# Kernel optimization log

Measured on AMD Instinct MI355X. Metric: run time of the kernel, lower is better.

## Reference

```python
import jax, jax.numpy as jnp
import numpy as np

N, M1, M2, D, S0, S1 = 60000, 40000, 40000, 64, 10, 20

def setup_inputs() -> dict:
    key = jax.random.key(0)
    ks = jax.random.split(key, 10)
    return {
        "h0": jax.random.normal(ks[0], (N, D), jnp.float32),
        "h1": jax.random.normal(ks[1], (M1, D), jnp.float32),
        "h2": jax.random.normal(ks[2], (M2, D), jnp.float32),
        "nei0": jax.random.randint(ks[3], (N, S0), 0, M1),
        "nei1": jax.random.randint(ks[4], (N, S1), 0, M2),
        "att_w0": jax.random.normal(ks[5], (1, 2 * D), jnp.float32) * 0.15,
        "att_w1": jax.random.normal(ks[6], (1, 2 * D), jnp.float32) * 0.15,
        "fc_w": jax.random.normal(ks[7], (D, D), jnp.float32) * 0.15,
        "fc_b": jnp.zeros((D,), jnp.float32),
        "fus_att_w": jax.random.normal(ks[8], (1, D), jnp.float32) * 0.15,
        "glob_att": jax.random.normal(ks[9], (1, D), jnp.float32) * 0.15,
        "gate": jnp.float32(0.8),
    }

def _nei_att(nei, h, h_refer, att_w):
    # F.embedding gather: [N, S, D]
    nei_emb = h[nei]
    d = h.shape[-1]
    # concat([h_refer, nei_emb]) @ att.T == h_refer@a_ref + nei_emb@a_nei
    a_ref, a_nei = att_w[0, :d], att_w[0, d:]
    scores = (h_refer @ a_ref)[:, None] + nei_emb @ a_nei  # [N, S]
    scores = jax.nn.leaky_relu(scores, 0.01)
    w = jax.nn.softmax(scores, axis=1)  # softmax over neighbors
    return jnp.einsum('ns,nsd->nd', w, nei_emb)

def reference(h0, h1, h2, nei0, nei1, att_w0, att_w1, fc_w, fc_b, fus_att_w, glob_att, gate):
    # intra (per neighbor type) attention + elu
    e0 = jax.nn.elu(_nei_att(nei0, h1, h0, att_w0))
    e1 = jax.nn.elu(_nei_att(nei1, h2, h0, att_w1))
    # fus_att (inter-type semantic attention)
    def beta_of(e):
        sp = jnp.tanh(e @ fc_w.T + fc_b)
        return (sp @ fus_att_w[0]).mean()
    beta = jax.nn.softmax(jnp.stack([beta_of(e0), beta_of(e1)]))
    z_mc = beta[0] * e0 + beta[1] * e1
    # global encoder: softmax over all nodes of all types
    all_nodes = jnp.concatenate([h0, h1, h2], axis=0)
    s = (all_nodes @ glob_att[0]) / jnp.sqrt(jnp.float32(D))
    w = jax.nn.softmax(s, axis=0)[:, None]
    global_embed = (w * all_nodes).sum(axis=0)  # [D]
    # weighted gate fusion
    gv = jax.nn.sigmoid(gate)
    return gv * z_mc + (1.0 - gv) * global_embed
```

## Files before the change

### kernel.cpp

```cpp
#include <hip/hip_runtime.h>
#include <math.h>

#define N_NODES 60000
#define M1_N    40000
#define M2_N    40000
#define DD      64
#define S0_N    10
#define S1_N    20
#define R_TOTAL (N_NODES + M1_N + M2_N)
#define T_H0    (N_NODES / 16)
#define T_H1    (T_H0 + M1_N / 16)
#define T_ALL   (T_H1 + M2_N / 16)
#define PROJ_GRID 1024
#define BETA_GRID 512

typedef __attribute__((ext_vector_type(8))) short short8;
typedef __attribute__((ext_vector_type(4))) float f32x4;

__device__ __forceinline__ float wave_sum(float x) {
#pragma unroll
    for (int o = 32; o >= 1; o >>= 1) x += __shfl_xor(x, o, 64);
    return x;
}
__device__ __forceinline__ float bcast(float v, int l) {
    return __uint_as_float(__builtin_amdgcn_readlane(__float_as_uint(v), l));
}
__device__ __forceinline__ float tanh_fast(float x) {
    return 1.f - 2.f / (__expf(2.f * x) + 1.f);
}
__device__ __forceinline__ unsigned short f2bf(float x) {
    unsigned u = __float_as_uint(x);
    return (unsigned short)((u + 0x7FFFu + ((u >> 16) & 1u)) >> 16);
}
__device__ __forceinline__ float bf2f(unsigned short u) {
    return __uint_as_float(((unsigned)u) << 16);
}

__global__ __launch_bounds__(256) void k_proj(
    const float* __restrict__ h0, const float* __restrict__ h1, const float* __restrict__ h2,
    const float* __restrict__ aw0, const float* __restrict__ aw1, const float* __restrict__ gatt,
    float* __restrict__ part,
    float* __restrict__ p0r0, float* __restrict__ p0r1,
    float* __restrict__ p1, float* __restrict__ p2,
    unsigned short* __restrict__ h1bf, unsigned short* __restrict__ h2bf)
{
    __shared__ float s_wsum[64];
    __shared__ float s_se;
    __shared__ float s_es[4][16];
    const int tid = threadIdx.x, lane = tid & 63, wid = tid >> 6;
    if (tid < 64) s_wsum[tid] = 0.f;
    if (tid == 0) s_se = 0.f;
    __syncthreads();

    const int m = lane & 15, quad = lane >> 4;

    short8 b0, b1;
    {
        const float* vsel = 0;
        if (m == 1) vsel = aw0;
        else if (m == 2) vsel = aw1;
        else if (m == 3) vsel = aw0 + DD;
        else if (m == 4) vsel = aw1 + DD;
        else if (m == 0) vsel = gatt;
#pragma unroll
        for (int j = 0; j < 8; j++) {
            b0[j] = vsel ? (short)f2bf(vsel[quad * 8 + j]) : (short)0;
            b1[j] = vsel ? (short)f2bf(vsel[32 + quad * 8 + j]) : (short)0;
        }
    }

    float wacc0[8], wacc1[8];
#pragma unroll
    for (int j = 0; j < 8; j++) { wacc0[j] = 0.f; wacc1[j] = 0.f; }
    float r_se = 0.f;

    const int gw = blockIdx.x * 4 + wid, nw = gridDim.x * 4;
    for (int tile = gw; tile < T_ALL; tile += nw) {
        const float* src; int rbase, region;
        if (tile < T_H0)      { src = h0; rbase = tile * 16;          region = 0; }
        else if (tile < T_H1) { src = h1; rbase = (tile - T_H0) * 16; region = 1; }
        else                  { src = h2; rbase = (tile - T_H1) * 16; region = 2; }
        const int row = rbase + m;
        const float4* rpa = (const float4*)(src + (size_t)row * DD + quad * 8);
        const float4* rpb = (const float4*)(src + (size_t)row * DD + 32 + quad * 8);
        const float4 va = rpa[0], vb = rpa[1];
        const float4 vc = rpb[0], vd = rpb[1];

        short8 a0, a1;
        a0[0] = (short)f2bf(va.x); a0[1] = (short)f2bf(va.y);
        a0[2] = (short)f2bf(va.z); a0[3] = (short)f2bf(va.w);
        a0[4] = (short)f2bf(vb.x); a0[5] = (short)f2bf(vb.y);
        a0[6] = (short)f2bf(vb.z); a0[7] = (short)f2bf(vb.w);
        a1[0] = (short)f2bf(vc.x); a1[1] = (short)f2bf(vc.y);
        a1[2] = (short)f2bf(vc.z); a1[3] = (short)f2bf(vc.w);
        a1[4] = (short)f2bf(vd.x); a1[5] = (short)f2bf(vd.y);
        a1[6] = (short)f2bf(vd.z); a1[7] = (short)f2bf(vd.w);

        f32x4 c = {0.f, 0.f, 0.f, 0.f};
        c = __builtin_amdgcn_mfma_f32_16x16x32_bf16(a0, b0, c, 0, 0, 0);
        c = __builtin_amdgcn_mfma_f32_16x16x32_bf16(a1, b1, c, 0, 0, 0);

        if (m == 0) {
            float4 e4;
            e4.x = __expf(c[0] * 0.125f); e4.y = __expf(c[1] * 0.125f);
            e4.z = __expf(c[2] * 0.125f); e4.w = __expf(c[3] * 0.125f);
            *(float4*)&s_es[wid][quad * 4] = e4;
        }
        __builtin_amdgcn_wave_barrier();
        const float es = s_es[wid][m];
        r_se += es;
        wacc0[0] = fmaf(es, va.x, wacc0[0]); wacc0[1] = fmaf(es, va.y, wacc0[1]);
        wacc0[2] = fmaf(es, va.z, wacc0[2]); wacc0[3] = fmaf(es, va.w, wacc0[3]);
        wacc0[4] = fmaf(es, vb.x, wacc0[4]); wacc0[5] = fmaf(es, vb.y, wacc0[5]);
        wacc0[6] = fmaf(es, vb.z, wacc0[6]); wacc0[7] = fmaf(es, vb.w, wacc0[7]);
        wacc1[0] = fmaf(es, vc.x, wacc1[0]); wacc1[1] = fmaf(es, vc.y, wacc1[1]);
        wacc1[2] = fmaf(es, vc.z, wacc1[2]); wacc1[3] = fmaf(es, vc.w, wacc1[3]);
        wacc1[4] = fmaf(es, vd.x, wacc1[4]); wacc1[5] = fmaf(es, vd.y, wacc1[5]);
        wacc1[6] = fmaf(es, vd.z, wacc1[6]); wacc1[7] = fmaf(es, vd.w, wacc1[7]);

        if (region == 0) {
            if (m == 1) { float4 t = {c[0], c[1], c[2], c[3]}; *(float4*)(p0r0 + rbase + quad * 4) = t; }
            if (m == 2) { float4 t = {c[0], c[1], c[2], c[3]}; *(float4*)(p0r1 + rbase + quad * 4) = t; }
        } else if (region == 1) {
            if (m == 3) { float4 t = {c[0], c[1], c[2], c[3]}; *(float4*)(p1 + rbase + quad * 4) = t; }
            *(short8*)(h1bf + (size_t)row * DD + quad * 8) = a0;
            *(short8*)(h1bf + (size_t)row * DD + 32 + quad * 8) = a1;
        } else {
            if (m == 4) { float4 t = {c[0], c[1], c[2], c[3]}; *(float4*)(p2 + rbase + quad * 4) = t; }
            *(short8*)(h2bf + (size_t)row * DD + quad * 8) = a0;
            *(short8*)(h2bf + (size_t)row * DD + 32 + quad * 8) = a1;
        }
    }

    r_se *= 0.25f;
#pragma unroll
    for (int o = 1; o <= 8; o <<= 1) {
#pragma unroll
        for (int j = 0; j < 8; j++) {
            wacc0[j] += __shfl_xor(wacc0[j], o, 64);
            wacc1[j] += __shfl_xor(wacc1[j], o, 64);
        }
    }
    if (m == 0) {
#pragma unroll
        for (int j = 0; j < 8; j++) {
            atomicAdd(&s_wsum[quad * 8 + j],      wacc0[j]);
            atomicAdd(&s_wsum[32 + quad * 8 + j], wacc1[j]);
        }
    }
    const float se = wave_sum(r_se);
    if (lane == 0) atomicAdd(&s_se, se);
    __syncthreads();
    if (tid < 64) part[tid * PROJ_GRID + blockIdx.x] = s_wsum[tid];
    if (tid == 64) part[64 * PROJ_GRID + blockIdx.x] = s_se;
}

__global__ __launch_bounds__(256) void k_attn(
    const unsigned short* __restrict__ h1bf, const unsigned short* __restrict__ h2bf,
    const int* __restrict__ nei0, const int* __restrict__ nei1,
    const float* __restrict__ p0r0, const float* __restrict__ p0r1,
    const float* __restrict__ p1, const float* __restrict__ p2,
    unsigned short* __restrict__ e0bf, unsigned short* __restrict__ e1bf)
{
    const int tid = threadIdx.x, lane = tid & 63, wid = tid >> 6;
    const bool grp0 = (lane < S0_N);
    const bool grp1 = (lane >= 32) && (lane < 32 + S1_N);
    const int gw = blockIdx.x * 4 + wid;
    const int nw = gridDim.x * 4;
    for (int n = gw; n < N_NODES; n += nw) {
        const float pr0 = p0r0[n];
        const float pr1 = p0r1[n];

        int idx = 0; float w = 0.f;
        if (grp0) idx = nei0[n * S0_N + lane];
        if (grp1) idx = nei1[n * S1_N + (lane - 32)];
        if (grp0 | grp1) {
            float t = (grp0 ? pr0 : pr1) + (grp0 ? p1[idx] : p2[idx]);
            t = (t >= 0.f) ? t : 0.01f * t;
            w = __expf(t);
        }
        float sv = w;
#pragma unroll
        for (int o = 16; o >= 1; o >>= 1) sv += __shfl_xor(sv, o, 64);
        const float inv0 = 1.f / bcast(sv, 0);
        const float inv1 = 1.f / bcast(sv, 32);

        float v0[S0_N], v1[S1_N];
#pragma unroll
        for (int s = 0; s < S0_N; s++) {
            const int i0 = __builtin_amdgcn_readlane(idx, s);
            v0[s] = bf2f(h1bf[i0 * DD + lane]);
        }
#pragma unroll
        for (int s = 0; s < S1_N; s++) {
            const int i1 = __builtin_amdgcn_readlane(idx, 32 + s);
            v1[s] = bf2f(h2bf[i1 * DD + lane]);
        }

        {
            float ea = 0.f, eb = 0.f;
#pragma unroll
            for (int s = 0; s < S0_N; s += 2) {
                ea = fmaf(bcast(w, s),     v0[s],     ea);
                eb = fmaf(bcast(w, s + 1), v0[s + 1], eb);
            }
            float e = (ea + eb) * inv0;
            e = (e > 0.f) ? e : (__expf(e) - 1.f);
            e0bf[n * DD + lane] = f2bf(e);
        }
        {
            float ea = 0.f, eb = 0.f, ec = 0.f, ed = 0.f;
#pragma unroll
            for (int s = 0; s < S1_N; s += 4) {
                ea = fmaf(bcast(w, 32 + s), v1[s],     ea);
                eb = fmaf(bcast(w, 33 + s), v1[s + 1], eb);
                ec = fmaf(bcast(w, 34 + s), v1[s + 2], ec);
                ed = fmaf(bcast(w, 35 + s), v1[s + 3], ed);
            }
            float e = ((ea + eb) + (ec + ed)) * inv1;
            e = (e > 0.f) ? e : (__expf(e) - 1.f);
            e1bf[n * DD + lane] = f2bf(e);
        }
    }
}

__global__ __launch_bounds__(256) void k_beta(
    const unsigned short* __restrict__ e0bf, const unsigned short* __restrict__ e1bf,
    const float* __restrict__ fcw, const float* __restrict__ fcb,
    const float* __restrict__ fus, float* __restrict__ bpart)
{
    __shared__ float s_part[2];
    const int tid = threadIdx.x, lane = tid & 63, wid = tid >> 6;
    if (tid < 2) s_part[tid] = 0.f;
    const int m = lane & 15, q = lane >> 4;

    short8 bfr[4][2];
    float fb[4], fu[4];
#pragma unroll
    for (int t = 0; t < 4; t++) {
        const float* wrow = fcw + (t * 16 + m) * DD;
#pragma unroll
        for (int h = 0; h < 2; h++) {
            const float* p = wrow + h * 32 + q * 8;
#pragma unroll
            for (int j = 0; j < 8; j++) bfr[t][h][j] = (short)f2bf(p[j]);
        }
        fb[t] = fcb[t * 16 + m];
        fu[t] = fus[t * 16 + m];
    }
    __syncthreads();

    float rb0 = 0.f, rb1 = 0.f;
    const int gw = blockIdx.x * 4 + wid;
    const int nw = gridDim.x * 4;
    for (int tile = gw; tile < N_NODES / 16; tile += nw) {
        const int rowbase = (tile * 16 + m) * DD + q * 8;
        {
            const short8 a0 = *(const short8*)(e0bf + rowbase);
            const short8 a1 = *(const short8*)(e0bf + rowbase + 32);
            f32x4 c[4];
#pragma unroll
            for (int t = 0; t < 4; t++) {
                c[t] = f32x4{0.f, 0.f, 0.f, 0.f};
                c[t] = __builtin_amdgcn_mfma_f32_16x16x32_bf16(a0, bfr[t][0], c[t], 0, 0, 0);
                c[t] = __builtin_amdgcn_mfma_f32_16x16x32_bf16(a1, bfr[t][1], c[t], 0, 0, 0);
            }
#pragma unroll
            for (int t = 0; t < 4; t++)
#pragma unroll
                for (int j = 0; j < 4; j++)
                    rb0 += tanh_fast(c[t][j] + fb[t]) * fu[t];
        }
        {
            const short8 a0 = *(const short8*)(e1bf + rowbase);
            const short8 a1 = *(const short8*)(e1bf + rowbase + 32);
            f32x4 c[4];
#pragma unroll
            for (int t = 0; t < 4; t++) {
                c[t] = f32x4{0.f, 0.f, 0.f, 0.f};
                c[t] = __builtin_amdgcn_mfma_f32_16x16x32_bf16(a0, bfr[t][0], c[t], 0, 0, 0);
                c[t] = __builtin_amdgcn_mfma_f32_16x16x32_bf16(a1, bfr[t][1], c[t], 0, 0, 0);
            }
#pragma unroll
            for (int t = 0; t < 4; t++)
#pragma unroll
                for (int j = 0; j < 4; j++)
                    rb1 += tanh_fast(c[t][j] + fb[t]) * fu[t];
        }
    }
    const float b0 = wave_sum(rb0);
    const float b1 = wave_sum(rb1);
    if (lane == 0) { atomicAdd(&s_part[0], b0); atomicAdd(&s_part[1], b1); }
    __syncthreads();
    if (tid == 0) {
        bpart[blockIdx.x]             = s_part[0];
        bpart[BETA_GRID + blockIdx.x] = s_part[1];
    }
}

__global__ __launch_bounds__(256) void k_reduce(
    const float* __restrict__ part, const float* __restrict__ bpart,
    float* __restrict__ accum)
{
    const int tid = threadIdx.x, lane = tid & 63, wid = tid >> 6;
    if (wid == 0) {
        float t0 = 0.f, t1 = 0.f;
#pragma unroll
        for (int k = 0; k < BETA_GRID / 64; k++) {
            t0 += bpart[lane + 64 * k];
            t1 += bpart[BETA_GRID + lane + 64 * k];
        }
        t0 = wave_sum(t0); t1 = wave_sum(t1);
        if (lane == 0) { accum[0] = t0; accum[1] = t1; }
    }
    for (int j = wid; j < 65; j += 4) {
        float s = 0.f;
#pragma unroll
        for (int k = 0; k < PROJ_GRID / 64; k++)
            s += part[j * PROJ_GRID + lane + 64 * k];
        s = wave_sum(s);
        if (lane == 0) {
            if (j < 64) accum[4 + j] = s;
            else        accum[2] = s;
        }
    }
}

__global__ __launch_bounds__(256) void k_out(
    const unsigned short* __restrict__ e0bf, const unsigned short* __restrict__ e1bf,
    const float* __restrict__ accum, const float* __restrict__ gate,
    float* __restrict__ out)
{
    const int i = blockIdx.x * 256 + threadIdx.x;
    const float b0 = accum[0] * (1.f / N_NODES);
    const float b1 = accum[1] * (1.f / N_NODES);
    const float mx = fmaxf(b0, b1);
    const float eb0 = __expf(b0 - mx), eb1 = __expf(b1 - mx);
    const float gv  = 1.f / (1.f + __expf(-gate[0]));
    const float c0  = gv * eb0 / (eb0 + eb1);
    const float c1  = gv * eb1 / (eb0 + eb1);
    const float cg  = (1.f - gv) / accum[2];

    const float4 av = ((const float4*)(accum + 4))[i & 15];
    const ushort4 ua = ((const ushort4*)e0bf)[i];
    const ushort4 ub = ((const ushort4*)e1bf)[i];
    float4 o;
    o.x = c0 * bf2f(ua.x) + c1 * bf2f(ub.x) + cg * av.x;
    o.y = c0 * bf2f(ua.y) + c1 * bf2f(ub.y) + cg * av.y;
    o.z = c0 * bf2f(ua.z) + c1 * bf2f(ub.z) + cg * av.z;
    o.w = c0 * bf2f(ua.w) + c1 * bf2f(ub.w) + cg * av.w;
    ((float4*)out)[i] = o;
}

extern "C" void kernel_launch(void* const* d_in, const int* in_sizes, int n_in,
                              void* d_out, int out_size, void* d_ws, size_t ws_size,
                              hipStream_t stream) {
    (void)in_sizes; (void)n_in; (void)out_size; (void)ws_size;
    const float* h0   = (const float*)d_in[0];
    const float* h1   = (const float*)d_in[1];
    const float* h2   = (const float*)d_in[2];
    const int*   nei0 = (const int*)  d_in[3];
    const int*   nei1 = (const int*)  d_in[4];
    const float* aw0  = (const float*)d_in[5];
    const float* aw1  = (const float*)d_in[6];
    const float* fcw  = (const float*)d_in[7];
    const float* fcb  = (const float*)d_in[8];
    const float* fus  = (const float*)d_in[9];
    const float* gatt = (const float*)d_in[10];
    const float* gate = (const float*)d_in[11];
    float* out = (float*)d_out;

    float* ws    = (float*)d_ws;
    float* accum = ws;
    float* p0r0  = ws + 256;
    float* p0r1  = p0r0 + N_NODES;
    float* p1    = p0r1 + N_NODES;
    float* p2    = p1 + M1_N;
    unsigned short* h1bf = (unsigned short*)(p2 + M2_N);
    unsigned short* h2bf = h1bf + (size_t)M1_N * DD;
    unsigned short* e0bf = h2bf + (size_t)M2_N * DD;
    unsigned short* e1bf = e0bf + (size_t)N_NODES * DD;
    float* part  = (float*)(e1bf + (size_t)N_NODES * DD);
    float* bpart = part + 65 * PROJ_GRID;

    k_proj<<<PROJ_GRID, 256, 0, stream>>>(h0, h1, h2, aw0, aw1, gatt, part,
                                          p0r0, p0r1, p1, p2, h1bf, h2bf);
    k_attn<<<2048, 256, 0, stream>>>(h1bf, h2bf, nei0, nei1, p0r0, p0r1, p1, p2, e0bf, e1bf);
    k_beta<<<BETA_GRID, 256, 0, stream>>>(e0bf, e1bf, fcw, fcb, fus, bpart);
    k_reduce<<<1, 256, 0, stream>>>(part, bpart, accum);
    k_out<<<(N_NODES * DD / 4) / 256, 256, 0, stream>>>(e0bf, e1bf, accum, gate, out);
}
```

Baseline: 176.9 us.

## Fuse beta projection into attention kernel via per-wave LDS tiles

Merges the separate semantic-attention (beta) kernel into the neighbour-attention kernel. Each wave now processes a 16-node tile, stages its bf16 e0/e1 rows in LDS and runs the MFMA fc projection plus tanh reduction directly. This removes the global re-read of e0bf/e1bf and one kernel launch. The h2/p2 gathers are also addressed through h1bf/p1 with an M1 offset, relying on the buffers being laid out contiguously in the workspace. In exchange the grid shrinks to 960 blocks and each wave loops serially over 16 nodes, which lowers the number of waves available to hide gather latency.

```diff
diff --git a/kernel.cpp b/kernel.cpp
--- a/kernel.cpp
+++ b/kernel.cpp
@@ -12,7 +12,8 @@
 #define T_H1    (T_H0 + M1_N / 16)
 #define T_ALL   (T_H1 + M2_N / 16)
 #define PROJ_GRID 1024
-#define BETA_GRID 512
+#define ATTN_GRID 960
+#define N_TILES  (N_NODES / 16)
 
 typedef __attribute__((ext_vector_type(8))) short short8;
 typedef __attribute__((ext_vector_type(4))) float f32x4;
@@ -156,136 +157,126 @@
 }
 
 __global__ __launch_bounds__(256) void k_attn(
-    const unsigned short* __restrict__ h1bf, const unsigned short* __restrict__ h2bf,
+    const unsigned short* __restrict__ h1bf,
     const int* __restrict__ nei0, const int* __restrict__ nei1,
     const float* __restrict__ p0r0, const float* __restrict__ p0r1,
-    const float* __restrict__ p1, const float* __restrict__ p2,
-    unsigned short* __restrict__ e0bf, unsigned short* __restrict__ e1bf)
+    const float* __restrict__ p1,
+    const float* __restrict__ fcw, const float* __restrict__ fcb,
+    const float* __restrict__ fus,
+    unsigned short* __restrict__ e0bf, unsigned short* __restrict__ e1bf,
+    float* __restrict__ bpart)
 {
-    const int tid = threadIdx.x, lane = tid & 63, wid = tid >> 6;
-    const bool grp0 = (lane < S0_N);
-    const bool grp1 = (lane >= 32) && (lane < 32 + S1_N);
-    const int gw = blockIdx.x * 4 + wid;
-    const int nw = gridDim.x * 4;
-    for (int n = gw; n < N_NODES; n += nw) {
-        const float pr0 = p0r0[n];
-        const float pr1 = p0r1[n];
-
-        int idx = 0; float w = 0.f;
-        if (grp0) idx = nei0[n * S0_N + lane];
-        if (grp1) idx = nei1[n * S1_N + (lane - 32)];
-        if (grp0 | grp1) {
-            float t = (grp0 ? pr0 : pr1) + (grp0 ? p1[idx] : p2[idx]);
-            t = (t >= 0.f) ? t : 0.01f * t;
-            w = __expf(t);
-        }
-        float sv = w;
-#pragma unroll
-        for (int o = 16; o >= 1; o >>= 1) sv += __shfl_xor(sv, o, 64);
-        const float inv0 = 1.f / bcast(sv, 0);
-        const float inv1 = 1.f / bcast(sv, 32);
-
-        float v0[S0_N], v1[S1_N];
-#pragma unroll
-        for (int s = 0; s < S0_N; s++) {
-            const int i0 = __builtin_amdgcn_readlane(idx, s);
-            v0[s] = bf2f(h1bf[i0 * DD + lane]);
-        }
-#pragma unroll
-        for (int s = 0; s < S1_N; s++) {
-            const int i1 = __builtin_amdgcn_readlane(idx, 32 + s);
-            v1[s] = bf2f(h2bf[i1 * DD + lane]);
-        }
-
-        {
-            float ea = 0.f, eb = 0.f;
-#pragma unroll
-            for (int s = 0; s < S0_N; s += 2) {
-                ea = fmaf(bcast(w, s),     v0[s],     ea);
-                eb = fmaf(bcast(w, s + 1), v0[s + 1], eb);
-            }
-            float e = (ea + eb) * inv0;
-            e = (e > 0.f) ? e : (__expf(e) - 1.f);
-            e0bf[n * DD + lane] = f2bf(e);
-        }
-        {
-            float ea = 0.f, eb = 0.f, ec = 0.f, ed = 0.f;
-#pragma unroll
-            for (int s = 0; s < S1_N; s += 4) {
-                ea = fmaf(bcast(w, 32 + s), v1[s],     ea);
-                eb = fmaf(bcast(w, 33 + s), v1[s + 1], eb);
-                ec = fmaf(bcast(w, 34 + s), v1[s + 2], ec);
-                ed = fmaf(bcast(w, 35 + s), v1[s + 3], ed);
-            }
-            float e = ((ea + eb) + (ec + ed)) * inv1;
-            e = (e > 0.f) ? e : (__expf(e) - 1.f);
-            e1bf[n * DD + lane] = f2bf(e);
-        }
-    }
-}
-
-__global__ __launch_bounds__(256) void k_beta(
-    const unsigned short* __restrict__ e0bf, const unsigned short* __restrict__ e1bf,
-    const float* __restrict__ fcw, const float* __restrict__ fcb,
-    const float* __restrict__ fus, float* __restrict__ bpart)
-{
+    __shared__ __align__(16) unsigned short s_et[4][2][16 * 88];
     __shared__ float s_part[2];
     const int tid = threadIdx.x, lane = tid & 63, wid = tid >> 6;
     if (tid < 2) s_part[tid] = 0.f;
-    const int m = lane & 15, q = lane >> 4;
+    const int m = lane & 15, quad = lane >> 4;
 
     short8 bfr[4][2];
     float fb[4], fu[4];
 #pragma unroll
-    for (int t = 0; t < 4; t++) {
-        const float* wrow = fcw + (t * 16 + m) * DD;
+    for (int t4 = 0; t4 < 4; t4++) {
+        const float* wrow = fcw + (t4 * 16 + m) * DD;
 #pragma unroll
         for (int h = 0; h < 2; h++) {
-            const float* p = wrow + h * 32 + q * 8;
-#pragma unroll
-            for (int j = 0; j < 8; j++) bfr[t][h][j] = (short)f2bf(p[j]);
-        }
-        fb[t] = fcb[t * 16 + m];
-        fu[t] = fus[t * 16 + m];
+            const float* p = wrow + h * 32 + quad * 8;
+#pragma unroll
+            for (int j = 0; j < 8; j++) bfr[t4][h][j] = (short)f2bf(p[j]);
+        }
+        fb[t4] = fcb[t4 * 16 + m];
+        fu[t4] = fus[t4 * 16 + m];
     }
     __syncthreads();
 
     float rb0 = 0.f, rb1 = 0.f;
-    const int gw = blockIdx.x * 4 + wid;
-    const int nw = gridDim.x * 4;
-    for (int tile = gw; tile < N_NODES / 16; tile += nw) {
-        const int rowbase = (tile * 16 + m) * DD + q * 8;
-        {
-            const short8 a0 = *(const short8*)(e0bf + rowbase);
-            const short8 a1 = *(const short8*)(e0bf + rowbase + 32);
+    const int t = blockIdx.x * 4 + wid;
+    if (t < N_TILES) {
+        const bool grp0 = (lane < S0_N);
+        const bool grp1 = (lane >= 32) && (lane < 32 + S1_N);
+#pragma unroll 1
+        for (int i = 0; i < 16; i++) {
+            const int n = t * 16 + i;
+            const float pr0 = p0r0[n];
+            const float pr1 = p0r1[n];
+
+            int idx = 0; float w = 0.f;
+            if (grp0) idx = nei0[n * S0_N + lane];
+            if (grp1) idx = nei1[n * S1_N + (lane - 32)] + M1_N;
+            if (grp0 | grp1) {
+                float sc = (grp0 ? pr0 : pr1) + p1[idx];
+                sc = (sc >= 0.f) ? sc : 0.01f * sc;
+                w = __expf(sc);
+            }
+
+            float v0[S0_N], v1[S1_N];
+#pragma unroll
+            for (int s = 0; s < S0_N; s++) {
+                const int i0 = __builtin_amdgcn_readlane(idx, s);
+                v0[s] = bf2f(h1bf[i0 * DD + lane]);
+            }
+#pragma unroll
+            for (int s = 0; s < S1_N; s++) {
+                const int i1 = __builtin_amdgcn_readlane(idx, 32 + s);
+                v1[s] = bf2f(h1bf[i1 * DD + lane]);
+            }
+
+            float sv = w;
+#pragma unroll
+            for (int o = 16; o >= 1; o >>= 1) sv += __shfl_xor(sv, o, 64);
+            const float inv0 = 1.f / bcast(sv, 0);
+            const float inv1 = 1.f / bcast(sv, 32);
+
+            float e0v, e1v;
+            {
+                float ea = 0.f, eb = 0.f;
+#pragma unroll
+                for (int s = 0; s < S0_N; s += 2) {
+                    ea = fmaf(bcast(w, s),     v0[s],     ea);
+                    eb = fmaf(bcast(w, s + 1), v0[s + 1], eb);
+                }
+                float e = (ea + eb) * inv0;
+                e0v = (e > 0.f) ? e : (__expf(e) - 1.f);
+            }
+            {
+                float ea = 0.f, eb = 0.f, ec = 0.f, ed = 0.f;
+#pragma unroll
+                for (int s = 0; s < S1_N; s += 4) {
+                    ea = fmaf(bcast(w, 32 + s), v1[s],     ea);
+                    eb = fmaf(bcast(w, 33 + s), v1[s + 1], eb);
+                    ec = fmaf(bcast(w, 34 + s), v1[s + 2], ec);
+                    ed = fmaf(bcast(w, 35 + s), v1[s + 3], ed);
+                }
+                float e = ((ea + eb) + (ec + ed)) * inv1;
+                e1v = (e > 0.f) ? e : (__expf(e) - 1.f);
+            }
+            const unsigned short bs0 = f2bf(e0v);
+            const unsigned short bs1 = f2bf(e1v);
+            e0bf[n * DD + lane] = bs0;
+            e1bf[n * DD + lane] = bs1;
+            s_et[wid][0][i * 88 + lane] = bs0;
+            s_et[wid][1][i * 88 + lane] = bs1;
+        }
+        __builtin_amdgcn_wave_barrier();
+
+#pragma unroll
+        for (int which = 0; which < 2; which++) {
+            const unsigned short* bp = &s_et[wid][which][m * 88 + quad * 8];
+            const short8 a0 = *(const short8*)bp;
+            const short8 a1 = *(const short8*)(bp + 32);
             f32x4 c[4];
 #pragma unroll
-            for (int t = 0; t < 4; t++) {
-                c[t] = f32x4{0.f, 0.f, 0.f, 0.f};
-                c[t] = __builtin_amdgcn_mfma_f32_16x16x32_bf16(a0, bfr[t][0], c[t], 0, 0, 0);
-                c[t] = __builtin_amdgcn_mfma_f32_16x16x32_bf16(a1, bfr[t][1], c[t], 0, 0, 0);
-            }
-#pragma unroll
-            for (int t = 0; t < 4; t++)
+            for (int t4 = 0; t4 < 4; t4++) {
+                c[t4] = f32x4{0.f, 0.f, 0.f, 0.f};
+                c[t4] = __builtin_amdgcn_mfma_f32_16x16x32_bf16(a0, bfr[t4][0], c[t4], 0, 0, 0);
+                c[t4] = __builtin_amdgcn_mfma_f32_16x16x32_bf16(a1, bfr[t4][1], c[t4], 0, 0, 0);
+            }
+            float r = 0.f;
+#pragma unroll
+            for (int t4 = 0; t4 < 4; t4++)
 #pragma unroll
                 for (int j = 0; j < 4; j++)
-                    rb0 += tanh_fast(c[t][j] + fb[t]) * fu[t];
-        }
-        {
-            const short8 a0 = *(const short8*)(e1bf + rowbase);
-            const short8 a1 = *(const short8*)(e1bf + rowbase + 32);
-            f32x4 c[4];
-#pragma unroll
-            for (int t = 0; t < 4; t++) {
-                c[t] = f32x4{0.f, 0.f, 0.f, 0.f};
-                c[t] = __builtin_amdgcn_mfma_f32_16x16x32_bf16(a0, bfr[t][0], c[t], 0, 0, 0);
-                c[t] = __builtin_amdgcn_mfma_f32_16x16x32_bf16(a1, bfr[t][1], c[t], 0, 0, 0);
-            }
-#pragma unroll
-            for (int t = 0; t < 4; t++)
-#pragma unroll
-                for (int j = 0; j < 4; j++)
-                    rb1 += tanh_fast(c[t][j] + fb[t]) * fu[t];
+                    r += tanh_fast(c[t4][j] + fb[t4]) * fu[t4];
+            if (which == 0) rb0 = r; else rb1 = r;
         }
     }
     const float b0 = wave_sum(rb0);
@@ -294,7 +285,7 @@
     __syncthreads();
     if (tid == 0) {
         bpart[blockIdx.x]             = s_part[0];
-        bpart[BETA_GRID + blockIdx.x] = s_part[1];
+        bpart[ATTN_GRID + blockIdx.x] = s_part[1];
     }
 }
 
@@ -306,9 +297,9 @@
     if (wid == 0) {
         float t0 = 0.f, t1 = 0.f;
 #pragma unroll
-        for (int k = 0; k < BETA_GRID / 64; k++) {
+        for (int k = 0; k < ATTN_GRID / 64; k++) {
             t0 += bpart[lane + 64 * k];
-            t1 += bpart[BETA_GRID + lane + 64 * k];
+            t1 += bpart[ATTN_GRID + lane + 64 * k];
         }
         t0 = wave_sum(t0); t1 = wave_sum(t1);
         if (lane == 0) { accum[0] = t0; accum[1] = t1; }
@@ -385,8 +376,8 @@
 
     k_proj<<<PROJ_GRID, 256, 0, stream>>>(h0, h1, h2, aw0, aw1, gatt, part,
                                           p0r0, p0r1, p1, p2, h1bf, h2bf);
-    k_attn<<<2048, 256, 0, stream>>>(h1bf, h2bf, nei0, nei1, p0r0, p0r1, p1, p2, e0bf, e1bf);
-    k_beta<<<BETA_GRID, 256, 0, stream>>>(e0bf, e1bf, fcw, fcb, fus, bpart);
+    k_attn<<<ATTN_GRID, 256, 0, stream>>>(h1bf, nei0, nei1, p0r0, p0r1, p1,
+                                          fcw, fcb, fus, e0bf, e1bf, bpart);
     k_reduce<<<1, 256, 0, stream>>>(part, bpart, accum);
     k_out<<<(N_NODES * DD / 4) / 256, 256, 0, stream>>>(e0bf, e1bf, accum, gate, out);
 }
```

Measured after the change: 196.6 us. 11.1% more time.

## Gather neighbor rows with 8-byte vector loads, four rows per wave instruction

Applied to the files above, without the earlier changes.

The attention kernel now splits each wave into four 16-lane groups. Each lane loads four bf16 values of one neighbor row at once, so one instruction fetches four rows, instead of one scalar bf16 per lane per neighbor. Weighted sums are built per group and combined with cross-group shuffles; group 0 writes e0 and group 1 writes e1 as ushort4 stores. It also treats h2bf and p2 as a tail of h1bf and p1 by offsetting nei1 indices by M1, which relies on the workspace keeping those buffers contiguous. The goal is fewer memory instructions and wider transactions in a latency-bound gather, at the cost of extra shuffles and padded zero-weight lanes.

```diff
diff --git a/kernel.cpp b/kernel.cpp
--- a/kernel.cpp
+++ b/kernel.cpp
@@ -156,13 +156,14 @@
 }
 
 __global__ __launch_bounds__(256) void k_attn(
-    const unsigned short* __restrict__ h1bf, const unsigned short* __restrict__ h2bf,
+    const unsigned short* __restrict__ h1bf,
     const int* __restrict__ nei0, const int* __restrict__ nei1,
     const float* __restrict__ p0r0, const float* __restrict__ p0r1,
-    const float* __restrict__ p1, const float* __restrict__ p2,
+    const float* __restrict__ p1,
     unsigned short* __restrict__ e0bf, unsigned short* __restrict__ e1bf)
 {
     const int tid = threadIdx.x, lane = tid & 63, wid = tid >> 6;
+    const int sub = lane & 15, grp = lane >> 4;
     const bool grp0 = (lane < S0_N);
     const bool grp1 = (lane >= 32) && (lane < 32 + S1_N);
     const int gw = blockIdx.x * 4 + wid;
@@ -173,53 +174,79 @@
 
         int idx = 0; float w = 0.f;
         if (grp0) idx = nei0[n * S0_N + lane];
-        if (grp1) idx = nei1[n * S1_N + (lane - 32)];
+        if (grp1) idx = nei1[n * S1_N + (lane - 32)] + M1_N;
         if (grp0 | grp1) {
-            float t = (grp0 ? pr0 : pr1) + (grp0 ? p1[idx] : p2[idx]);
-            t = (t >= 0.f) ? t : 0.01f * t;
-            w = __expf(t);
-        }
+            float sc = (grp0 ? pr0 : pr1) + p1[idx];
+            sc = (sc >= 0.f) ? sc : 0.01f * sc;
+            w = __expf(sc);
+        }
+
+        int r0[3], r1[5];
+#pragma unroll
+        for (int j = 0; j < 3; j++) r0[j] = __shfl(idx, 4 * j + grp, 64);
+#pragma unroll
+        for (int j = 0; j < 5; j++) r1[j] = __shfl(idx, 32 + 4 * j + grp, 64);
+
+        ushort4 u0[3], u1[5];
+#pragma unroll
+        for (int j = 0; j < 3; j++)
+            u0[j] = *(const ushort4*)(h1bf + r0[j] * DD + 4 * sub);
+#pragma unroll
+        for (int j = 0; j < 5; j++)
+            u1[j] = *(const ushort4*)(h1bf + r1[j] * DD + 4 * sub);
+
         float sv = w;
 #pragma unroll
         for (int o = 16; o >= 1; o >>= 1) sv += __shfl_xor(sv, o, 64);
         const float inv0 = 1.f / bcast(sv, 0);
         const float inv1 = 1.f / bcast(sv, 32);
 
-        float v0[S0_N], v1[S1_N];
-#pragma unroll
-        for (int s = 0; s < S0_N; s++) {
-            const int i0 = __builtin_amdgcn_readlane(idx, s);
-            v0[s] = bf2f(h1bf[i0 * DD + lane]);
-        }
-#pragma unroll
-        for (int s = 0; s < S1_N; s++) {
-            const int i1 = __builtin_amdgcn_readlane(idx, 32 + s);
-            v1[s] = bf2f(h2bf[i1 * DD + lane]);
-        }
-
-        {
-            float ea = 0.f, eb = 0.f;
-#pragma unroll
-            for (int s = 0; s < S0_N; s += 2) {
-                ea = fmaf(bcast(w, s),     v0[s],     ea);
-                eb = fmaf(bcast(w, s + 1), v0[s + 1], eb);
-            }
-            float e = (ea + eb) * inv0;
-            e = (e > 0.f) ? e : (__expf(e) - 1.f);
-            e0bf[n * DD + lane] = f2bf(e);
-        }
-        {
-            float ea = 0.f, eb = 0.f, ec = 0.f, ed = 0.f;
-#pragma unroll
-            for (int s = 0; s < S1_N; s += 4) {
-                ea = fmaf(bcast(w, 32 + s), v1[s],     ea);
-                eb = fmaf(bcast(w, 33 + s), v1[s + 1], eb);
-                ec = fmaf(bcast(w, 34 + s), v1[s + 2], ec);
-                ed = fmaf(bcast(w, 35 + s), v1[s + 3], ed);
-            }
-            float e = ((ea + eb) + (ec + ed)) * inv1;
-            e = (e > 0.f) ? e : (__expf(e) - 1.f);
-            e1bf[n * DD + lane] = f2bf(e);
+        float w0[3], w1[5];
+#pragma unroll
+        for (int j = 0; j < 3; j++) w0[j] = __shfl(w, 4 * j + grp, 64);
+#pragma unroll
+        for (int j = 0; j < 5; j++) w1[j] = __shfl(w, 32 + 4 * j + grp, 64);
+
+        float4 a0 = make_float4(0.f, 0.f, 0.f, 0.f);
+#pragma unroll
+        for (int j = 0; j < 3; j++) {
+            a0.x = fmaf(w0[j], bf2f(u0[j].x), a0.x);
+            a0.y = fmaf(w0[j], bf2f(u0[j].y), a0.y);
+            a0.z = fmaf(w0[j], bf2f(u0[j].z), a0.z);
+            a0.w = fmaf(w0[j], bf2f(u0[j].w), a0.w);
+        }
+        float4 a1 = make_float4(0.f, 0.f, 0.f, 0.f);
+#pragma unroll
+        for (int j = 0; j < 5; j++) {
+            a1.x = fmaf(w1[j], bf2f(u1[j].x), a1.x);
+            a1.y = fmaf(w1[j], bf2f(u1[j].y), a1.y);
+            a1.z = fmaf(w1[j], bf2f(u1[j].z), a1.z);
+            a1.w = fmaf(w1[j], bf2f(u1[j].w), a1.w);
+        }
+#pragma unroll
+        for (int o = 16; o <= 32; o <<= 1) {
+            a0.x += __shfl_xor(a0.x, o, 64); a0.y += __shfl_xor(a0.y, o, 64);
+            a0.z += __shfl_xor(a0.z, o, 64); a0.w += __shfl_xor(a0.w, o, 64);
+            a1.x += __shfl_xor(a1.x, o, 64); a1.y += __shfl_xor(a1.y, o, 64);
+            a1.z += __shfl_xor(a1.z, o, 64); a1.w += __shfl_xor(a1.w, o, 64);
+        }
+        float4 e0v, e1v;
+        e0v.x = a0.x * inv0; e0v.y = a0.y * inv0; e0v.z = a0.z * inv0; e0v.w = a0.w * inv0;
+        e1v.x = a1.x * inv1; e1v.y = a1.y * inv1; e1v.z = a1.z * inv1; e1v.w = a1.w * inv1;
+        e0v.x = (e0v.x > 0.f) ? e0v.x : (__expf(e0v.x) - 1.f);
+        e0v.y = (e0v.y > 0.f) ? e0v.y : (__expf(e0v.y) - 1.f);
+        e0v.z = (e0v.z > 0.f) ? e0v.z : (__expf(e0v.z) - 1.f);
+        e0v.w = (e0v.w > 0.f) ? e0v.w : (__expf(e0v.w) - 1.f);
+        e1v.x = (e1v.x > 0.f) ? e1v.x : (__expf(e1v.x) - 1.f);
+        e1v.y = (e1v.y > 0.f) ? e1v.y : (__expf(e1v.y) - 1.f);
+        e1v.z = (e1v.z > 0.f) ? e1v.z : (__expf(e1v.z) - 1.f);
+        e1v.w = (e1v.w > 0.f) ? e1v.w : (__expf(e1v.w) - 1.f);
+        if (grp == 0) {
+            ushort4 s; s.x = f2bf(e0v.x); s.y = f2bf(e0v.y); s.z = f2bf(e0v.z); s.w = f2bf(e0v.w);
+            *(ushort4*)(e0bf + n * DD + 4 * sub) = s;
+        } else if (grp == 1) {
+            ushort4 s; s.x = f2bf(e1v.x); s.y = f2bf(e1v.y); s.z = f2bf(e1v.z); s.w = f2bf(e1v.w);
+            *(ushort4*)(e1bf + n * DD + 4 * sub) = s;
         }
     }
 }
@@ -385,7 +412,7 @@
 
     k_proj<<<PROJ_GRID, 256, 0, stream>>>(h0, h1, h2, aw0, aw1, gatt, part,
                                           p0r0, p0r1, p1, p2, h1bf, h2bf);
-    k_attn<<<2048, 256, 0, stream>>>(h1bf, h2bf, nei0, nei1, p0r0, p0r1, p1, p2, e0bf, e1bf);
+    k_attn<<<2048, 256, 0, stream>>>(h1bf, nei0, nei1, p0r0, p0r1, p1, e0bf, e1bf);
     k_beta<<<BETA_GRID, 256, 0, stream>>>(e0bf, e1bf, fcw, fcb, fus, bpart);
     k_reduce<<<1, 256, 0, stream>>>(part, bpart, accum);
     k_out<<<(N_NODES * DD / 4) / 256, 256, 0, stream>>>(e0bf, e1bf, accum, gate, out);
```

After: 176.1 us. About the same (-0.5%).
